# Performance work log

Hardware: AMD Instinct MI355X
Metric: run time of the kernel (lower is better)

## Reference

```python
import jax, jax.numpy as jnp
import numpy as np

N = 50000   # nodes
E = 500000  # edges
G = 64      # graphs in batch
H = 2       # attention heads
D = 64      # hidden per head (hid)
F_IN = 4    # num_features
C = 5       # num_classes
NEG_SLOPE = 0.2


def setup_inputs() -> dict:
    key = jax.random.key(0)
    ks = jax.random.split(key, 24)
    inp = {
        'x': jax.random.normal(ks[0], (N, F_IN), jnp.float32),
        'edge_index': jax.random.randint(ks[1], (2, E), 0, N, dtype=jnp.int64),
        'batch': jnp.sort(jax.random.randint(ks[2], (N,), 0, G, dtype=jnp.int64)),
    }
    ins = [F_IN, H * D, H * D, H * D]
    ki = 3
    for l, fin in enumerate(ins, 1):
        s = 1.0 / np.sqrt(fin)
        inp[f'W{l}'] = s * jax.random.normal(ks[ki], (fin, H * D), jnp.float32); ki += 1
        inp[f'asrc{l}'] = 0.1 * jax.random.normal(ks[ki], (H, D), jnp.float32); ki += 1
        inp[f'adst{l}'] = 0.1 * jax.random.normal(ks[ki], (H, D), jnp.float32); ki += 1
        inp[f'b{l}'] = 0.01 * jax.random.normal(ks[ki], (H * D,), jnp.float32); ki += 1
    inp['lin_w'] = (1.0 / np.sqrt(H * D)) * jax.random.normal(ks[ki], (H * D, C), jnp.float32); ki += 1
    inp['lin_b'] = jnp.zeros((C,), jnp.float32)
    return inp


def gat_conv(x, src, dst, W, a_src, a_dst, b):
    # x: [N, Fin] -> h: [N, H, D]
    h = (x @ W).reshape(-1, H, D)
    alpha_src = jnp.sum(h * a_src, axis=-1)  # [N, H]
    alpha_dst = jnp.sum(h * a_dst, axis=-1)  # [N, H]
    e = jax.nn.leaky_relu(alpha_src[src] + alpha_dst[dst], NEG_SLOPE)  # [E, H]
    # segment softmax over incoming edges of each dst node
    e_max = jax.ops.segment_max(e, dst, num_segments=N)  # [N, H]
    e_exp = jnp.exp(e - e_max[dst])
    denom = jax.ops.segment_sum(e_exp, dst, num_segments=N)
    alpha = e_exp / (denom[dst] + 1e-16)  # [E, H]
    msg = h[src] * alpha[:, :, None]  # [E, H, D]
    out = jax.ops.segment_sum(msg, dst, num_segments=N)  # [N, H, D]
    return out.reshape(-1, H * D) + b


def reference(x, edge_index, batch,
              W1, asrc1, adst1, b1,
              W2, asrc2, adst2, b2,
              W3, asrc3, adst3, b3,
              W4, asrc4, adst4, b4,
              lin_w, lin_b):
    src, dst = edge_index[0], edge_index[1]
    h = jax.nn.relu(gat_conv(x, src, dst, W1, asrc1, adst1, b1))
    h = jax.nn.relu(gat_conv(h, src, dst, W2, asrc2, adst2, b2))
    h = jax.nn.relu(gat_conv(h, src, dst, W3, asrc3, adst3, b3))
    h = jax.nn.relu(gat_conv(h, src, dst, W4, asrc4, adst4, b4))
    # global mean pool over graphs
    sums = jax.ops.segment_sum(h, batch, num_segments=G)  # [G, 128]
    counts = jax.ops.segment_sum(jnp.ones((h.shape[0],), h.dtype), batch, num_segments=G)
    pooled = sums / jnp.maximum(counts, 1.0)[:, None]
    return jax.nn.sigmoid(pooled @ lin_w + lin_b)  # [G, C]
```

## Files before the change

kernel.cpp:

```cpp
#include <hip/hip_runtime.h>
#include <math.h>

#define NHEAD 2
#define NDIM  64
#define HD    128
#define NGRAPH 64
#define NCLS  5
#define NEG_SLOPE 0.2f

typedef __attribute__((ext_vector_type(8))) short bf16x8;
typedef __attribute__((ext_vector_type(4))) float f32x4;

static __device__ __forceinline__ unsigned short f2bf(float f) {
    unsigned int u = __float_as_uint(f);
    u = (u + 0x7fff + ((u >> 16) & 1)) >> 16;
    return (unsigned short)u;
}
static __device__ __forceinline__ float bf2f(unsigned short b) {
    return __uint_as_float((unsigned int)b << 16);
}


__global__ void k_deg(const int* __restrict__ dst, int* __restrict__ deg, int E) {
    int i = blockIdx.x * blockDim.x + threadIdx.x;
    if (i < E) atomicAdd(&deg[dst[i]], 1);
}

__global__ __launch_bounds__(256) void k_scan_local(const int* __restrict__ deg,
                                                    int* __restrict__ ptr,
                                                    int* __restrict__ bsum, int n) {
    __shared__ int wsum[4];
    const int tid = threadIdx.x, lane = tid & 63, wid = tid >> 6;
    const int base = blockIdx.x * 2048 + tid * 8;
    int v[8];
    #pragma unroll
    for (int k = 0; k < 8; ++k) {
        int i = base + k;
        v[k] = (i < n) ? deg[i] : 0;
    }
    #pragma unroll
    for (int k = 1; k < 8; ++k) v[k] += v[k - 1];
    int x = v[7];
    #pragma unroll
    for (int off = 1; off < 64; off <<= 1) {
        int t = __shfl_up(x, off, 64);
        if (lane >= off) x += t;
    }
    if (lane == 63) wsum[wid] = x;
    __syncthreads();
    int woff = 0;
    #pragma unroll
    for (int k = 0; k < 4; ++k) woff += (k < wid) ? wsum[k] : 0;
    int texcl = woff + x - v[7];
    #pragma unroll
    for (int k = 0; k < 8; ++k) {
        int i = base + k;
        if (i < n) ptr[i + 1] = texcl + v[k];
    }
    if (tid == 255) bsum[blockIdx.x] = woff + x;
    if (blockIdx.x == 0 && tid == 0) ptr[0] = 0;
}

__global__ void k_scan_bsum(int* __restrict__ bsum, int B) {
    int lane = threadIdx.x;
    int carry = 0;
    for (int base = 0; base < B; base += 64) {
        int i = base + lane;
        int v = (i < B) ? bsum[i] : 0;
        int x = v;
        #pragma unroll
        for (int off = 1; off < 64; off <<= 1) {
            int t = __shfl_up(x, off, 64);
            if (lane >= off) x += t;
        }
        if (i < B) bsum[i] = carry + x - v;
        carry += __shfl(x, 63, 64);
    }
}

__global__ __launch_bounds__(256) void k_scan_add(int* __restrict__ ptr,
                                                  const int* __restrict__ bsum, int n) {
    int off = bsum[blockIdx.x];
    if (off == 0) return;
    const int base = blockIdx.x * 2048 + threadIdx.x * 8;
    #pragma unroll
    for (int k = 0; k < 8; ++k) {
        int i = base + k;
        if (i < n) ptr[i + 1] += off;
    }
}

__global__ void k_scatter(const int* __restrict__ src, const int* __restrict__ dst,
                          const int* __restrict__ ptr, int* __restrict__ fill,
                          int* __restrict__ csr, int E) {
    int i = blockIdx.x * blockDim.x + threadIdx.x;
    if (i < E) {
        int d = dst[i];
        int pos = atomicAdd(&fill[d], 1);
        csr[ptr[d] + pos] = src[i];
    }
}


__global__ void k_prepw(const float* __restrict__ W2, const float* __restrict__ W3,
                        const float* __restrict__ W4, unsigned short* __restrict__ Wt) {
    int idx = blockIdx.x * blockDim.x + threadIdx.x;
    if (idx >= 3 * HD * HD) return;
    int l = idx / (HD * HD), rem = idx % (HD * HD);
    int n = rem >> 7, k = rem & 127;
    const float* W = (l == 0) ? W2 : (l == 1) ? W3 : W4;
    Wt[idx] = f2bf(W[k * HD + n]);
}


__global__ void k_gemm1(const float* __restrict__ x, const float* __restrict__ W,
                        unsigned short* __restrict__ out, int N) {
    int idx = blockIdx.x * blockDim.x + threadIdx.x;
    if (idx >= N * HD) return;
    int node = idx >> 7, col = idx & 127;
    float4 xv = *(const float4*)&x[node * 4];
    float v = xv.x * W[col] + xv.y * W[128 + col] + xv.z * W[256 + col] + xv.w * W[384 + col];
    out[idx] = f2bf(v);
}

#define LDA 136
__global__ __launch_bounds__(256) void k_gemm_mfma(const unsigned short* __restrict__ A,
                                                   const unsigned short* __restrict__ Wt,
                                                   const float* __restrict__ asrc,
                                                   const float* __restrict__ adst,
                                                   unsigned short* __restrict__ out,
                                                   float* __restrict__ oas,
                                                   float* __restrict__ oad, int N) {
    __shared__ unsigned short As[128 * LDA];
    __shared__ unsigned short Ws[128 * LDA];
    const int tid = threadIdx.x;
    const int nbase = blockIdx.x * 128;
    const int lane = tid & 63, w = tid >> 6;
    const int l15 = lane & 15, quad = lane >> 4;
    const int koff = quad * 8;

    for (int c = tid; c < 2048; c += 256) {
        int row = c >> 4, k8 = (c & 15) << 3;
        int g = nbase + row;
        uint4 v = make_uint4(0, 0, 0, 0);
        if (g < N) v = *(const uint4*)&A[(size_t)g * HD + k8];
        *(uint4*)&As[row * LDA + k8] = v;
    }
    for (int c = tid; c < 2048; c += 256) {
        int row = c >> 4, k8 = (c & 15) << 3;
        *(uint4*)&Ws[row * LDA + k8] = *(const uint4*)&Wt[row * HD + k8];
    }
    float av[8], dv[8];
    #pragma unroll
    for (int c = 0; c < 8; ++c) {
        av[c] = asrc[c * 16 + l15];
        dv[c] = adst[c * 16 + l15];
    }
    __syncthreads();

    f32x4 acc0[8], acc1[8];
    #pragma unroll
    for (int c = 0; c < 8; ++c) { acc0[c] = (f32x4)(0.f); acc1[c] = (f32x4)(0.f); }

    const int r0 = w * 32 + l15;
    #pragma unroll
    for (int ks = 0; ks < 4; ++ks) {
        bf16x8 a0 = *(const bf16x8*)&As[r0 * LDA + ks * 32 + koff];
        bf16x8 a1 = *(const bf16x8*)&As[(r0 + 16) * LDA + ks * 32 + koff];
        #pragma unroll
        for (int c = 0; c < 8; ++c) {
            bf16x8 b = *(const bf16x8*)&Ws[(c * 16 + l15) * LDA + ks * 32 + koff];
            acc0[c] = __builtin_amdgcn_mfma_f32_16x16x32_bf16(a0, b, acc0[c], 0, 0, 0);
            acc1[c] = __builtin_amdgcn_mfma_f32_16x16x32_bf16(a1, b, acc1[c], 0, 0, 0);
        }
    }

    #pragma unroll
    for (int i = 0; i < 2; ++i) {
        int rowb = nbase + w * 32 + i * 16 + quad * 4;
        #pragma unroll
        for (int c = 0; c < 8; ++c) {
            f32x4 v = i ? acc1[c] : acc0[c];
            int col = c * 16 + l15;
            #pragma unroll
            for (int r = 0; r < 4; ++r) {
                int row = rowb + r;
                if (row < N) out[(size_t)row * HD + col] = f2bf(v[r]);
            }
        }
        #pragma unroll
        for (int r = 0; r < 4; ++r) {
            float ps0 = 0.f, ps1 = 0.f, pd0 = 0.f, pd1 = 0.f;
            #pragma unroll
            for (int c = 0; c < 4; ++c) {
                float hv = i ? acc1[c][r] : acc0[c][r];
                ps0 += hv * av[c]; pd0 += hv * dv[c];
            }
            #pragma unroll
            for (int c = 4; c < 8; ++c) {
                float hv = i ? acc1[c][r] : acc0[c][r];
                ps1 += hv * av[c]; pd1 += hv * dv[c];
            }
            #pragma unroll
            for (int off = 1; off < 16; off <<= 1) {
                ps0 += __shfl_xor(ps0, off);
                ps1 += __shfl_xor(ps1, off);
                pd0 += __shfl_xor(pd0, off);
                pd1 += __shfl_xor(pd1, off);
            }
            int row = rowb + r;
            if (l15 == 0 && row < N) {
                *(float2*)&oas[row * 2] = make_float2(ps0, ps1);
                *(float2*)&oad[row * 2] = make_float2(pd0, pd1);
            }
        }
    }
}

__global__ void k_alpha(const unsigned short* __restrict__ h, const float* __restrict__ asrc,
                        const float* __restrict__ adst, float* __restrict__ oas,
                        float* __restrict__ oad, int N) {
    int n = (blockIdx.x * blockDim.x + threadIdx.x) >> 6;
    int lane = threadIdx.x & 63;
    if (n >= N) return;
    ushort2 uv = *(const ushort2*)&h[(size_t)n * HD + lane * 2];
    float vx = bf2f(uv.x), vy = bf2f(uv.y);
    float2 av = *(const float2*)&asrc[lane * 2];
    float2 dv = *(const float2*)&adst[lane * 2];
    float s = vx * av.x + vy * av.y;
    float t = vx * dv.x + vy * dv.y;
    #pragma unroll
    for (int off = 16; off > 0; off >>= 1) {
        s += __shfl_xor(s, off);
        t += __shfl_xor(t, off);
    }
    if ((lane & 31) == 0) {
        int head = lane >> 5;
        oas[n * 2 + head] = s;
        oad[n * 2 + head] = t;
    }
}

__global__ void k_agg(const unsigned short* __restrict__ h, const float* __restrict__ oas,
                      const float* __restrict__ oad, const int* __restrict__ ptr,
                      const int* __restrict__ csr, const float* __restrict__ bias,
                      unsigned short* __restrict__ out, int N) {
    int n = (blockIdx.x * blockDim.x + threadIdx.x) >> 6;
    int lane = threadIdx.x & 63;
    if (n >= N) return;
    int beg = ptr[n], end = ptr[n + 1];
    if (beg == end) {
        float2 b2 = *(const float2*)&bias[lane * 2];
        unsigned int packed = (unsigned int)f2bf(fmaxf(b2.x, 0.f)) |
                              ((unsigned int)f2bf(fmaxf(b2.y, 0.f)) << 16);
        *(unsigned int*)&out[(size_t)n * HD + lane * 2] = packed;
        return;
    }
    const int quad = lane >> 4, sub = lane & 15;
    const int hsel = sub >> 3;
    float2 adn = *(const float2*)&oad[n * 2];
    float m0 = -INFINITY, m1 = -INFINITY, l0 = 0.f, l1 = 0.f;
    float acc[8];
    #pragma unroll
    for (int k = 0; k < 8; ++k) acc[k] = 0.f;

    for (int cbeg = beg; cbeg < end; cbeg += 64) {
        int cnt = min(64, end - cbeg);
        int s = 0;
        float e0 = -INFINITY, e1 = -INFINITY;
        if (lane < cnt) {
            s = csr[cbeg + lane];
            float2 as = *(const float2*)&oas[s * 2];
            e0 = as.x + adn.x; e0 = (e0 >= 0.f) ? e0 : NEG_SLOPE * e0;
            e1 = as.y + adn.y; e1 = (e1 >= 0.f) ? e1 : NEG_SLOPE * e1;
        }
        float c0 = e0, c1 = e1;
        #pragma unroll
        for (int off = 32; off > 0; off >>= 1) {
            c0 = fmaxf(c0, __shfl_xor(c0, off));
            c1 = fmaxf(c1, __shfl_xor(c1, off));
        }
        float nm0 = fmaxf(m0, c0), nm1 = fmaxf(m1, c1);
        float sc0 = __expf(m0 - nm0), sc1 = __expf(m1 - nm1);
        float p0 = (lane < cnt) ? __expf(e0 - nm0) : 0.f;
        float p1 = (lane < cnt) ? __expf(e1 - nm1) : 0.f;
        float s0 = p0, s1 = p1;
        #pragma unroll
        for (int off = 32; off > 0; off >>= 1) {
            s0 += __shfl_xor(s0, off);
            s1 += __shfl_xor(s1, off);
        }
        l0 = l0 * sc0 + s0;
        l1 = l1 * sc1 + s1;
        m0 = nm0; m1 = nm1;
        float scl = hsel ? sc1 : sc0;
        #pragma unroll
        for (int k = 0; k < 8; ++k) acc[k] *= scl;

        for (int j = 0; j < cnt; j += 4) {
            int jq = j + quad;
            int sj = __shfl(s, jq);
            float pa = __shfl(p0, jq);
            float pb = __shfl(p1, jq);
            float pj = hsel ? pb : pa;
            uint4 hv = *(const uint4*)&h[(size_t)sj * HD + sub * 8];
            #pragma unroll
            for (int k = 0; k < 4; ++k) {
                unsigned int u = (&hv.x)[k];
                acc[2 * k]     += pj * __uint_as_float(u << 16);
                acc[2 * k + 1] += pj * __uint_as_float(u & 0xffff0000u);
            }
        }
    }
    #pragma unroll
    for (int k = 0; k < 8; ++k) {
        acc[k] += __shfl_xor(acc[k], 16);
        acc[k] += __shfl_xor(acc[k], 32);
    }
    if (quad == 0) {
        float lsel = hsel ? l1 : l0;
        float inv = 1.f / (lsel + 1e-16f);
        float4 ba = *(const float4*)&bias[sub * 8];
        float4 bb = *(const float4*)&bias[sub * 8 + 4];
        float o[8];
        o[0] = fmaxf(acc[0] * inv + ba.x, 0.f);
        o[1] = fmaxf(acc[1] * inv + ba.y, 0.f);
        o[2] = fmaxf(acc[2] * inv + ba.z, 0.f);
        o[3] = fmaxf(acc[3] * inv + ba.w, 0.f);
        o[4] = fmaxf(acc[4] * inv + bb.x, 0.f);
        o[5] = fmaxf(acc[5] * inv + bb.y, 0.f);
        o[6] = fmaxf(acc[6] * inv + bb.z, 0.f);
        o[7] = fmaxf(acc[7] * inv + bb.w, 0.f);
        uint4 pk;
        pk.x = (unsigned int)f2bf(o[0]) | ((unsigned int)f2bf(o[1]) << 16);
        pk.y = (unsigned int)f2bf(o[2]) | ((unsigned int)f2bf(o[3]) << 16);
        pk.z = (unsigned int)f2bf(o[4]) | ((unsigned int)f2bf(o[5]) << 16);
        pk.w = (unsigned int)f2bf(o[6]) | ((unsigned int)f2bf(o[7]) << 16);
        *(uint4*)&out[(size_t)n * HD + sub * 8] = pk;
    }
}

__global__ void k_pool(const unsigned short* __restrict__ feat, const int* __restrict__ batch,
                       float* __restrict__ pooled, int* __restrict__ gcount, int N) {
    int col = threadIdx.x;
    int n0 = blockIdx.x * 128;
    int n1 = min(n0 + 128, N);
    float acc = 0.f;
    int curg = -1, runlen = 0;
    for (int n = n0; n < n1; ++n) {
        int g = batch[n];
        if (g != curg) {
            if (curg >= 0) {
                atomicAdd(&pooled[curg * HD + col], acc);
                if (col == 0) atomicAdd(&gcount[curg], runlen);
            }
            acc = 0.f; runlen = 0;
            curg = g;
        }
        acc += bf2f(feat[(size_t)n * HD + col]);
        runlen++;
    }
    if (curg >= 0) {
        atomicAdd(&pooled[curg * HD + col], acc);
        if (col == 0) atomicAdd(&gcount[curg], runlen);
    }
}

__global__ void k_final(const float* __restrict__ pooled, const int* __restrict__ gcount,
                        const float* __restrict__ lw, const float* __restrict__ lb,
                        float* __restrict__ out) {
    int tid = threadIdx.x;
    if (tid >= NGRAPH * NCLS) return;
    int g = tid / NCLS, c = tid % NCLS;
    float cnt = fmaxf((float)gcount[g], 1.f);
    const float* p = pooled + g * HD;
    float sum = 0.f;
    for (int k = 0; k < HD; ++k)
        sum += p[k] * lw[k * NCLS + c];
    float z = lb[c] + sum / cnt;
    out[tid] = 1.f / (1.f + __expf(-z));
}


static inline size_t al256(size_t x) { return (x + 255) & ~(size_t)255; }

extern "C" void kernel_launch(void* const* d_in, const int* in_sizes, int n_in,
                              void* d_out, int out_size, void* d_ws, size_t ws_size,
                              hipStream_t stream) {
    const int N = in_sizes[0] / 4;
    const int E = in_sizes[1] / 2;

    const float* x     = (const float*)d_in[0];
    const int*   esrc  = (const int*)d_in[1];
    const int*   edst  = esrc + E;
    const int*   batch = (const int*)d_in[2];
    const float* Wl[4]  = {(const float*)d_in[3],  (const float*)d_in[7],
                           (const float*)d_in[11], (const float*)d_in[15]};
    const float* asr[4] = {(const float*)d_in[4],  (const float*)d_in[8],
                           (const float*)d_in[12], (const float*)d_in[16]};
    const float* ads[4] = {(const float*)d_in[5],  (const float*)d_in[9],
                           (const float*)d_in[13], (const float*)d_in[17]};
    const float* bs[4]  = {(const float*)d_in[6],  (const float*)d_in[10],
                           (const float*)d_in[14], (const float*)d_in[18]};
    const float* lin_w = (const float*)d_in[19];
    const float* lin_b = (const float*)d_in[20];
    float* out = (float*)d_out;

    char* w = (char*)d_ws;
    size_t off = 0;
    auto alloc = [&](size_t bytes) -> void* {
        void* p = w + off;
        off = al256(off + bytes);
        return p;
    };
    int*   deg    = (int*)alloc((size_t)N * 4);
    int*   fill   = (int*)alloc((size_t)N * 4);
    int*   gcount = (int*)alloc((size_t)NGRAPH * 4);
    float* pooled = (float*)alloc((size_t)NGRAPH * HD * 4);
    size_t zbytes = off;
    int*   ptr    = (int*)alloc((size_t)(N + 1) * 4);
    int*   bsum   = (int*)alloc((size_t)1024 * 4);
    int*   csr    = (int*)alloc((size_t)E * 4);
    unsigned short* hbuf = (unsigned short*)alloc((size_t)N * HD * 2);
    unsigned short* feat = (unsigned short*)alloc((size_t)N * HD * 2);
    unsigned short* Wt   = (unsigned short*)alloc((size_t)3 * HD * HD * 2);
    float* a_src  = (float*)alloc((size_t)N * 2 * 4);
    float* a_dst  = (float*)alloc((size_t)N * 2 * 4);
    (void)ws_size; (void)n_in; (void)out_size;

    hipMemsetAsync(d_ws, 0, zbytes, stream);

    k_prepw<<<(3 * HD * HD + 255) / 256, 256, 0, stream>>>(Wl[1], Wl[2], Wl[3], Wt);
    k_deg<<<(E + 255) / 256, 256, 0, stream>>>(edst, deg, E);
    const int SB = (N + 2047) / 2048;
    k_scan_local<<<SB, 256, 0, stream>>>(deg, ptr, bsum, N);
    k_scan_bsum<<<1, 64, 0, stream>>>(bsum, SB);
    k_scan_add<<<SB, 256, 0, stream>>>(ptr, bsum, N);
    k_scatter<<<(E + 255) / 256, 256, 0, stream>>>(esrc, edst, ptr, fill, csr, E);

    const int node_wave_blocks = (N + 3) / 4;

    for (int layer = 0; layer < 4; ++layer) {
        if (layer == 0) {
            k_gemm1<<<(N * HD + 255) / 256, 256, 0, stream>>>(x, Wl[0], hbuf, N);
            k_alpha<<<node_wave_blocks, 256, 0, stream>>>(hbuf, asr[0], ads[0], a_src, a_dst, N);
        } else {
            k_gemm_mfma<<<(N + 127) / 128, 256, 0, stream>>>(
                feat, Wt + (size_t)(layer - 1) * HD * HD,
                asr[layer], ads[layer], hbuf, a_src, a_dst, N);
        }
        k_agg<<<node_wave_blocks, 256, 0, stream>>>(hbuf, a_src, a_dst, ptr, csr, bs[layer], feat, N);
    }

    k_pool<<<(N + 127) / 128, 128, 0, stream>>>(feat, batch, pooled, gcount, N);
    k_final<<<1, 320, 0, stream>>>(pooled, gcount, lin_w, lin_b, out);
}
```

Measured before the change: 406.1 us.

## Fuse layer-1 GEMM with alpha, pre-gather source logits, unroll aggregation by two

Layer 1's tiny GEMM and its attention-logit computation are merged into one kernel, with the logits taken from fp32 values before bf16 rounding, which removes a launch and a re-read of h. A new per-edge kernel gathers alpha_src into CSR order so that k_agg reads it contiguously instead of through a random index. The inner aggregation loop now processes two neighbour rows per step, putting more loads in flight. The trade-off is an extra 4 MB edge buffer and an extra kernel launch per layer, and the random gather still happens, just in a separate pass.

Result: slower. 414.8 us (+2.2%).

```diff
diff --git a/kernel.cpp b/kernel.cpp
--- a/kernel.cpp
+++ b/kernel.cpp
@@ -113,14 +113,37 @@
 }
 
 
-__global__ void k_gemm1(const float* __restrict__ x, const float* __restrict__ W,
-                        unsigned short* __restrict__ out, int N) {
-    int idx = blockIdx.x * blockDim.x + threadIdx.x;
-    if (idx >= N * HD) return;
-    int node = idx >> 7, col = idx & 127;
-    float4 xv = *(const float4*)&x[node * 4];
-    float v = xv.x * W[col] + xv.y * W[128 + col] + xv.z * W[256 + col] + xv.w * W[384 + col];
-    out[idx] = f2bf(v);
+__global__ void k_gemm1a(const float* __restrict__ x, const float* __restrict__ W,
+                         const float* __restrict__ asrc, const float* __restrict__ adst,
+                         unsigned short* __restrict__ out,
+                         float* __restrict__ oas, float* __restrict__ oad, int N) {
+    int n = (blockIdx.x * blockDim.x + threadIdx.x) >> 6;
+    int lane = threadIdx.x & 63;
+    if (n >= N) return;
+    float4 xv = *(const float4*)&x[n * 4];
+    int c0 = lane * 2;
+    float2 w0 = *(const float2*)&W[c0];
+    float2 w1 = *(const float2*)&W[128 + c0];
+    float2 w2 = *(const float2*)&W[256 + c0];
+    float2 w3 = *(const float2*)&W[384 + c0];
+    float v0 = xv.x * w0.x + xv.y * w1.x + xv.z * w2.x + xv.w * w3.x;
+    float v1 = xv.x * w0.y + xv.y * w1.y + xv.z * w2.y + xv.w * w3.y;
+    unsigned int pk = (unsigned int)f2bf(v0) | ((unsigned int)f2bf(v1) << 16);
+    *(unsigned int*)&out[(size_t)n * HD + c0] = pk;
+    float2 av = *(const float2*)&asrc[c0];
+    float2 dv = *(const float2*)&adst[c0];
+    float s = v0 * av.x + v1 * av.y;
+    float t = v0 * dv.x + v1 * dv.y;
+    #pragma unroll
+    for (int off = 16; off > 0; off >>= 1) {
+        s += __shfl_xor(s, off);
+        t += __shfl_xor(t, off);
+    }
+    if ((lane & 31) == 0) {
+        int head = lane >> 5;
+        oas[n * 2 + head] = s;
+        oad[n * 2 + head] = t;
+    }
 }
 
 #define LDA 136
@@ -217,31 +240,16 @@
     }
 }
 
-__global__ void k_alpha(const unsigned short* __restrict__ h, const float* __restrict__ asrc,
-                        const float* __restrict__ adst, float* __restrict__ oas,
-                        float* __restrict__ oad, int N) {
-    int n = (blockIdx.x * blockDim.x + threadIdx.x) >> 6;
-    int lane = threadIdx.x & 63;
-    if (n >= N) return;
-    ushort2 uv = *(const ushort2*)&h[(size_t)n * HD + lane * 2];
-    float vx = bf2f(uv.x), vy = bf2f(uv.y);
-    float2 av = *(const float2*)&asrc[lane * 2];
-    float2 dv = *(const float2*)&adst[lane * 2];
-    float s = vx * av.x + vy * av.y;
-    float t = vx * dv.x + vy * dv.y;
-    #pragma unroll
-    for (int off = 16; off > 0; off >>= 1) {
-        s += __shfl_xor(s, off);
-        t += __shfl_xor(t, off);
-    }
-    if ((lane & 31) == 0) {
-        int head = lane >> 5;
-        oas[n * 2 + head] = s;
-        oad[n * 2 + head] = t;
-    }
-}
-
-__global__ void k_agg(const unsigned short* __restrict__ h, const float* __restrict__ oas,
+__global__ void k_gatheras(const float* __restrict__ oas, const int* __restrict__ csr,
+                           float2* __restrict__ as_csr, int E) {
+    int i = blockIdx.x * blockDim.x + threadIdx.x;
+    if (i < E) {
+        int s = csr[i];
+        as_csr[i] = *(const float2*)&oas[s * 2];
+    }
+}
+
+__global__ void k_agg(const unsigned short* __restrict__ h, const float2* __restrict__ as_csr,
                       const float* __restrict__ oad, const int* __restrict__ ptr,
                       const int* __restrict__ csr, const float* __restrict__ bias,
                       unsigned short* __restrict__ out, int N) {
@@ -270,7 +278,7 @@
         float e0 = -INFINITY, e1 = -INFINITY;
         if (lane < cnt) {
             s = csr[cbeg + lane];
-            float2 as = *(const float2*)&oas[s * 2];
+            float2 as = as_csr[cbeg + lane];
             e0 = as.x + adn.x; e0 = (e0 >= 0.f) ? e0 : NEG_SLOPE * e0;
             e1 = as.y + adn.y; e1 = (e1 >= 0.f) ? e1 : NEG_SLOPE * e1;
         }
@@ -297,18 +305,24 @@
         #pragma unroll
         for (int k = 0; k < 8; ++k) acc[k] *= scl;
 
-        for (int j = 0; j < cnt; j += 4) {
-            int jq = j + quad;
-            int sj = __shfl(s, jq);
-            float pa = __shfl(p0, jq);
-            float pb = __shfl(p1, jq);
-            float pj = hsel ? pb : pa;
-            uint4 hv = *(const uint4*)&h[(size_t)sj * HD + sub * 8];
+        for (int j = 0; j < cnt; j += 8) {
+            int jq0 = j + quad, jq1 = j + quad + 4;
+            int sa = __shfl(s, jq0);
+            int sb = __shfl(s, jq1);
+            float pa0 = __shfl(p0, jq0);
+            float pa1 = __shfl(p1, jq0);
+            float pb0 = __shfl(p0, jq1);
+            float pb1 = __shfl(p1, jq1);
+            float pa = hsel ? pa1 : pa0;
+            float pb = hsel ? pb1 : pb0;
+            uint4 hva = *(const uint4*)&h[(size_t)sa * HD + sub * 8];
+            uint4 hvb = *(const uint4*)&h[(size_t)sb * HD + sub * 8];
             #pragma unroll
             for (int k = 0; k < 4; ++k) {
-                unsigned int u = (&hv.x)[k];
-                acc[2 * k]     += pj * __uint_as_float(u << 16);
-                acc[2 * k + 1] += pj * __uint_as_float(u & 0xffff0000u);
+                unsigned int ua = (&hva.x)[k];
+                unsigned int ub = (&hvb.x)[k];
+                acc[2 * k]     += pa * __uint_as_float(ua << 16) + pb * __uint_as_float(ub << 16);
+                acc[2 * k + 1] += pa * __uint_as_float(ua & 0xffff0000u) + pb * __uint_as_float(ub & 0xffff0000u);
             }
         }
     }
@@ -424,8 +438,9 @@
     unsigned short* hbuf = (unsigned short*)alloc((size_t)N * HD * 2);
     unsigned short* feat = (unsigned short*)alloc((size_t)N * HD * 2);
     unsigned short* Wt   = (unsigned short*)alloc((size_t)3 * HD * HD * 2);
-    float* a_src  = (float*)alloc((size_t)N * 2 * 4);
-    float* a_dst  = (float*)alloc((size_t)N * 2 * 4);
+    float*  a_src  = (float*)alloc((size_t)N * 2 * 4);
+    float*  a_dst  = (float*)alloc((size_t)N * 2 * 4);
+    float2* as_csr = (float2*)alloc((size_t)E * 8);
     (void)ws_size; (void)n_in; (void)out_size;
 
     hipMemsetAsync(d_ws, 0, zbytes, stream);
@@ -439,17 +454,19 @@
     k_scatter<<<(E + 255) / 256, 256, 0, stream>>>(esrc, edst, ptr, fill, csr, E);
 
     const int node_wave_blocks = (N + 3) / 4;
+    const int edge_blocks = (E + 255) / 256;
 
     for (int layer = 0; layer < 4; ++layer) {
         if (layer == 0) {
-            k_gemm1<<<(N * HD + 255) / 256, 256, 0, stream>>>(x, Wl[0], hbuf, N);
-            k_alpha<<<node_wave_blocks, 256, 0, stream>>>(hbuf, asr[0], ads[0], a_src, a_dst, N);
+            k_gemm1a<<<node_wave_blocks, 256, 0, stream>>>(
+                x, Wl[0], asr[0], ads[0], hbuf, a_src, a_dst, N);
         } else {
             k_gemm_mfma<<<(N + 127) / 128, 256, 0, stream>>>(
                 feat, Wt + (size_t)(layer - 1) * HD * HD,
                 asr[layer], ads[layer], hbuf, a_src, a_dst, N);
         }
-        k_agg<<<node_wave_blocks, 256, 0, stream>>>(hbuf, a_src, a_dst, ptr, csr, bs[layer], feat, N);
+        k_gatheras<<<edge_blocks, 256, 0, stream>>>(a_src, csr, as_csr, E);
+        k_agg<<<node_wave_blocks, 256, 0, stream>>>(hbuf, as_csr, a_dst, ptr, csr, bs[layer], feat, N);
     }
 
     k_pool<<<(N + 127) / 128, 128, 0, stream>>>(feat, batch, pooled, gcount, N);
```
